# Performance work log

Hardware: AMD Instinct MI355X
Metric: run time of the kernel (lower is better)

The kernel has to match this reference:

```python
import jax, jax.numpy as jnp
import numpy as np

B = 16384       # batch of weight blocks
IN = 64         # input_size == e_dim
DENC = 512      # dim_encoder
NRES = 2        # n_resblock (weights shared, see ResidualStack [block]*n)
NE = 2048       # n_embeddings
P = 12          # basis vectors per block
BETA = 0.25
SCALE = 1.0
SHIFT = 0.0


def setup_inputs() -> dict:
    key = jax.random.key(0)
    ks = jax.random.split(key, 6)
    s = 0.02
    return {
        "x": jax.random.normal(ks[0], (B, IN), dtype=jnp.float32),
        "enc_w1": jax.random.normal(ks[1], (IN, DENC), dtype=jnp.float32) * s,
        "enc_b1": jnp.zeros((DENC,), jnp.float32),
        "res_w": jax.random.normal(ks[2], (DENC, DENC), dtype=jnp.float32) * s,
        "res_b": jnp.zeros((DENC,), jnp.float32),
        "res_g": jnp.ones((DENC,), jnp.float32),
        "res_beta": jnp.zeros((DENC,), jnp.float32),
        "enc_w2": jax.random.normal(ks[3], (DENC, IN * P), dtype=jnp.float32) * s,
        "enc_b2": jnp.zeros((IN * P,), jnp.float32),
        "emb": jax.random.uniform(ks[4], (NE, IN), jnp.float32, -1.0 / NE, 1.0 / NE),
    }


def _layer_norm(r, g, b):
    mu = jnp.mean(r, axis=-1, keepdims=True)
    var = jnp.mean((r - mu) ** 2, axis=-1, keepdims=True)
    return (r - mu) * jax.lax.rsqrt(var + 1e-5) * g + b


def reference(x, enc_w1, enc_b1, res_w, res_b, res_g, res_beta, enc_w2, enc_b2, emb):
    sg = jax.lax.stop_gradient
    x_shift = (x - SHIFT) / SCALE

    # encoder: Linear -> (shared ResBlock) x NRES -> Linear
    h = x_shift @ enc_w1 + enc_b1                      # (B, DENC)
    for _ in range(NRES):
        h = h + jax.nn.relu(_layer_norm(h @ res_w + res_b, res_g, res_beta))
    z = h @ enc_w2 + enc_b2                            # (B, P*IN)

    z_e = z.reshape(B, P, IN)
    zf = z_e.reshape(-1, IN)                           # (B*P, IN)

    # pairwise squared distances to codebook, argmin, gather
    d = (jnp.sum(zf ** 2, axis=1, keepdims=True)
         + jnp.sum(emb ** 2, axis=1)
         - 2.0 * zf @ emb.T)                           # (B*P, NE)
    idx = jnp.argmin(d, axis=1)                        # (B*P,)
    z_q = emb[idx].reshape(B, P, IN)

    loss = (jnp.mean((sg(z_q) - z_e) ** 2)
            + BETA * jnp.mean((z_q - sg(z_e)) ** 2))

    # straight-through estimator
    z_q = z_e + sg(z_q - z_e)

    counts = jnp.zeros((NE,), jnp.float32).at[idx].add(1.0) / idx.shape[0]
    perplexity = jnp.exp(-jnp.sum(counts * jnp.log(counts + 1e-10)))

    # pinv-based reconstruction: A (B, IN, P), coeff = pinv(A) @ x_shift
    A = jnp.transpose(z_q, (0, 2, 1))                  # (B, IN, P)
    coeff = jnp.matmul(jnp.linalg.pinv(A), x_shift[..., None])  # (B, P, 1)
    x_hat = jnp.matmul(A, coeff)[..., 0]               # (B, IN)
    x_hat = SCALE * x_hat + SHIFT

    return (loss, x_hat, perplexity, idx, coeff)
```

## Files before the change

kernel.cpp:

```cpp
#include <hip/hip_runtime.h>
#include <math.h>

#define B_    16384
#define IN_   64
#define DENC_ 512
#define NE_   2048
#define P_    12
#define ROWS_ 196608
#define BETA_ 0.25

#define XHAT_OFF 1
#define PERP_OFF 1048577
#define IDXF_OFF 1048578
#define COEF_OFF 1245186

typedef __bf16 bf16x8 __attribute__((ext_vector_type(8)));
typedef float  f32x16 __attribute__((ext_vector_type(16)));

__device__ __forceinline__ void split3(float v, __bf16& h, __bf16& m, __bf16& l) {
    h = (__bf16)v;
    float r1 = v - (float)h;
    m = (__bf16)r1;
    float r2 = r1 - (float)m;
    l = (__bf16)r2;
}

__global__ void k_wsplit(const float* __restrict__ W,
                         __bf16* __restrict__ Wh, __bf16* __restrict__ Wm,
                         __bf16* __restrict__ Wl, int kshift, int N, int total) {
    int idx = blockIdx.x * 256 + threadIdx.x;
    if (idx < total) {
        int n = idx >> kshift;
        int k = idx & ((1 << kshift) - 1);
        float v = W[(size_t)k * N + n];
        __bf16 h, m, l;
        split3(v, h, m, l);
        Wh[idx] = h; Wm[idx] = m; Wl[idx] = l;
    }
}

__global__ __launch_bounds__(256) void k_gemm_mfma(const float* __restrict__ A,
                                                   const __bf16* __restrict__ Bh,
                                                   const __bf16* __restrict__ Bm,
                                                   const __bf16* __restrict__ Bl,
                                                   const float* __restrict__ bias,
                                                   float* __restrict__ C,
                                                   int N, int K) {
    __shared__ __bf16 eS[3][64 * 64];

    const int tid = threadIdx.x;
    const int w = tid >> 6, lane = tid & 63;
    const int r0 = blockIdx.y * 128 + w * 32;
    const int n0 = blockIdx.x * 64;
    const int lrow = lane & 31;
    const int half = lane >> 5;

    f32x16 acc0, acc1;
#pragma unroll
    for (int i = 0; i < 16; ++i) { acc0[i] = 0.0f; acc1[i] = 0.0f; }

    for (int k0 = 0; k0 < K; k0 += 64) {
        __syncthreads();
        {
            const int col = tid >> 3, q = tid & 7;
#pragma unroll
            for (int p = 0; p < 2; ++p) {
                int cc = col + 32 * p;
                int g = q ^ (cc & 7);
                size_t soff = (size_t)(n0 + cc) * K + k0 + q * 8;
                int doff = cc * 64 + g * 8;
                *(float4*)(&eS[0][doff]) = *(const float4*)(Bh + soff);
                *(float4*)(&eS[1][doff]) = *(const float4*)(Bm + soff);
                *(float4*)(&eS[2][doff]) = *(const float4*)(Bl + soff);
            }
        }
        __syncthreads();

        bf16x8 ah[4], am[4], al[4];
        {
            const float* ar = A + (size_t)(r0 + lrow) * K + k0 + half * 8;
#pragma unroll
            for (int kc = 0; kc < 4; ++kc) {
                float4 u0 = *(const float4*)(ar + kc * 16);
                float4 u1 = *(const float4*)(ar + kc * 16 + 4);
                float v[8] = {u0.x, u0.y, u0.z, u0.w, u1.x, u1.y, u1.z, u1.w};
#pragma unroll
                for (int j = 0; j < 8; ++j) {
                    __bf16 hh, mm, ll;
                    split3(v[j], hh, mm, ll);
                    ah[kc][j] = hh; am[kc][j] = mm; al[kc][j] = ll;
                }
            }
        }

#pragma unroll
        for (int kc = 0; kc < 4; ++kc) {
            const int q = kc * 2 + half;
            const int g = (q ^ (lrow & 7)) * 8;
            bf16x8 b0h = *(const bf16x8*)(&eS[0][lrow * 64 + g]);
            bf16x8 b0m = *(const bf16x8*)(&eS[1][lrow * 64 + g]);
            bf16x8 b0l = *(const bf16x8*)(&eS[2][lrow * 64 + g]);
            bf16x8 b1h = *(const bf16x8*)(&eS[0][(lrow + 32) * 64 + g]);
            bf16x8 b1m = *(const bf16x8*)(&eS[1][(lrow + 32) * 64 + g]);
            bf16x8 b1l = *(const bf16x8*)(&eS[2][(lrow + 32) * 64 + g]);

            acc0 = __builtin_amdgcn_mfma_f32_32x32x16_bf16(ah[kc], b0h, acc0, 0, 0, 0);
            acc1 = __builtin_amdgcn_mfma_f32_32x32x16_bf16(ah[kc], b1h, acc1, 0, 0, 0);
            acc0 = __builtin_amdgcn_mfma_f32_32x32x16_bf16(ah[kc], b0m, acc0, 0, 0, 0);
            acc1 = __builtin_amdgcn_mfma_f32_32x32x16_bf16(ah[kc], b1m, acc1, 0, 0, 0);
            acc0 = __builtin_amdgcn_mfma_f32_32x32x16_bf16(am[kc], b0h, acc0, 0, 0, 0);
            acc1 = __builtin_amdgcn_mfma_f32_32x32x16_bf16(am[kc], b1h, acc1, 0, 0, 0);
            acc0 = __builtin_amdgcn_mfma_f32_32x32x16_bf16(ah[kc], b0l, acc0, 0, 0, 0);
            acc1 = __builtin_amdgcn_mfma_f32_32x32x16_bf16(ah[kc], b1l, acc1, 0, 0, 0);
            acc0 = __builtin_amdgcn_mfma_f32_32x32x16_bf16(am[kc], b0m, acc0, 0, 0, 0);
            acc1 = __builtin_amdgcn_mfma_f32_32x32x16_bf16(am[kc], b1m, acc1, 0, 0, 0);
            acc0 = __builtin_amdgcn_mfma_f32_32x32x16_bf16(al[kc], b0h, acc0, 0, 0, 0);
            acc1 = __builtin_amdgcn_mfma_f32_32x32x16_bf16(al[kc], b1h, acc1, 0, 0, 0);
        }
    }

    const int col0 = n0 + lrow, col1 = col0 + 32;
    const float bv0 = bias[col0], bv1 = bias[col1];
#pragma unroll
    for (int r = 0; r < 16; ++r) {
        int row = r0 + (r & 3) + 8 * (r >> 2) + 4 * half;
        C[(size_t)row * N + col0] = acc0[r] + bv0;
        C[(size_t)row * N + col1] = acc1[r] + bv1;
    }
}

__global__ __launch_bounds__(256) void k_lnrelu(const float* __restrict__ t,
                                                float* __restrict__ h,
                                                const float* __restrict__ g,
                                                const float* __restrict__ beta) {
    const int tid = threadIdx.x;
    const int wv = tid >> 6, lane = tid & 63;
    const int row = blockIdx.x * 4 + wv;
    const float* tr = t + (size_t)row * DENC_;
    float* hr = h + (size_t)row * DENC_;

    float4 v0 = *(const float4*)(tr + lane * 4);
    float4 v1 = *(const float4*)(tr + 256 + lane * 4);

    float s = v0.x + v0.y + v0.z + v0.w + v1.x + v1.y + v1.z + v1.w;
#pragma unroll
    for (int m = 1; m < 64; m <<= 1) s += __shfl_xor(s, m);
    float mu = s / 512.0f;

    float d0x = v0.x - mu, d0y = v0.y - mu, d0z = v0.z - mu, d0w = v0.w - mu;
    float d1x = v1.x - mu, d1y = v1.y - mu, d1z = v1.z - mu, d1w = v1.w - mu;
    float vs = d0x * d0x + d0y * d0y + d0z * d0z + d0w * d0w +
               d1x * d1x + d1y * d1y + d1z * d1z + d1w * d1w;
#pragma unroll
    for (int m = 1; m < 64; m <<= 1) vs += __shfl_xor(vs, m);
    float var = vs / 512.0f;
    float rs = (float)(1.0 / sqrt((double)var + 1e-5));

    float4 g0 = *(const float4*)(g + lane * 4);
    float4 g1 = *(const float4*)(g + 256 + lane * 4);
    float4 b0 = *(const float4*)(beta + lane * 4);
    float4 b1 = *(const float4*)(beta + 256 + lane * 4);

    float4 h0 = *(float4*)(hr + lane * 4);
    float4 h1 = *(float4*)(hr + 256 + lane * 4);

    h0.x += fmaxf(d0x * rs * g0.x + b0.x, 0.0f);
    h0.y += fmaxf(d0y * rs * g0.y + b0.y, 0.0f);
    h0.z += fmaxf(d0z * rs * g0.z + b0.z, 0.0f);
    h0.w += fmaxf(d0w * rs * g0.w + b0.w, 0.0f);
    h1.x += fmaxf(d1x * rs * g1.x + b1.x, 0.0f);
    h1.y += fmaxf(d1y * rs * g1.y + b1.y, 0.0f);
    h1.z += fmaxf(d1z * rs * g1.z + b1.z, 0.0f);
    h1.w += fmaxf(d1w * rs * g1.w + b1.w, 0.0f);

    *(float4*)(hr + lane * 4) = h0;
    *(float4*)(hr + 256 + lane * 4) = h1;
}

__global__ void k_esplit(const float* __restrict__ emb, float* __restrict__ se,
                         __bf16* __restrict__ Ehi, __bf16* __restrict__ Emid,
                         __bf16* __restrict__ Elo) {
    int c = blockIdx.x * 256 + threadIdx.x;
    if (c < NE_) {
        float s = 0.0f;
        for (int k = 0; k < 64; ++k) {
            float v = emb[(size_t)c * 64 + k];
            s += v * v;
            __bf16 h, m, l;
            split3(v, h, m, l);
            Ehi[(size_t)c * 64 + k] = h;
            Emid[(size_t)c * 64 + k] = m;
            Elo[(size_t)c * 64 + k] = l;
        }
        se[c] = s;
    }
}

__global__ __launch_bounds__(256) void k_rowsq(const float* __restrict__ z,
                                               float* __restrict__ sz) {
    const int tid = threadIdx.x;
    const int row = blockIdx.x * 64 + (tid >> 2);
    const int part = tid & 3;
    const float4* zp = (const float4*)(z + (size_t)row * 64) + part * 4;
    float s = 0.0f;
#pragma unroll
    for (int i = 0; i < 4; ++i) {
        float4 v = zp[i];
        s += v.x * v.x + v.y * v.y + v.z * v.z + v.w * v.w;
    }
    s += __shfl_xor(s, 1);
    s += __shfl_xor(s, 2);
    if (part == 0) sz[row] = s;
}

__global__ __launch_bounds__(256) void k_distm(const float* __restrict__ z,
                                               const float* __restrict__ se,
                                               const float* __restrict__ sz,
                                               const __bf16* __restrict__ Ehi,
                                               const __bf16* __restrict__ Emid,
                                               const __bf16* __restrict__ Elo,
                                               int* __restrict__ idxw,
                                               float* __restrict__ idxf,
                                               float* __restrict__ dminw,
                                               int* __restrict__ counts) {
    __shared__ __bf16 eS[3][64 * 64];

    const int tid = threadIdx.x;
    const int w = tid >> 6, lane = tid & 63;
    const int r0 = blockIdx.x * 128 + w * 32;
    const int lrow = lane & 31;
    const int half = lane >> 5;

    bf16x8 ah[4], am[4], al[4];
    {
        const float* zr = z + (size_t)(r0 + lrow) * 64 + half * 8;
#pragma unroll
        for (int kc = 0; kc < 4; ++kc) {
            float4 u0 = *(const float4*)(zr + kc * 16);
            float4 u1 = *(const float4*)(zr + kc * 16 + 4);
            float v[8] = {u0.x, u0.y, u0.z, u0.w, u1.x, u1.y, u1.z, u1.w};
#pragma unroll
            for (int j = 0; j < 8; ++j) {
                __bf16 hh, mm, ll;
                split3(v[j], hh, mm, ll);
                ah[kc][j] = hh; am[kc][j] = mm; al[kc][j] = ll;
            }
        }
    }

    float szv[16];
#pragma unroll
    for (int r = 0; r < 16; ++r) {
        int rl = (r & 3) + 8 * (r >> 2) + 4 * half;
        szv[r] = sz[r0 + rl];
    }

    float bd[16];
    int bi[16];
#pragma unroll
    for (int r = 0; r < 16; ++r) { bd[r] = 1e30f; bi[r] = 0; }

    for (int ch = 0; ch < 32; ++ch) {
        const int c0 = ch * 64;
        __syncthreads();
        {
            const int col = tid >> 3, q = tid & 7;
#pragma unroll
            for (int p = 0; p < 2; ++p) {
                int cc = col + 32 * p;
                int g = q ^ (cc & 7);
                size_t soff = (size_t)(c0 + cc) * 64 + q * 8;
                int doff = cc * 64 + g * 8;
                *(float4*)(&eS[0][doff]) = *(const float4*)(Ehi + soff);
                *(float4*)(&eS[1][doff]) = *(const float4*)(Emid + soff);
                *(float4*)(&eS[2][doff]) = *(const float4*)(Elo + soff);
            }
        }
        __syncthreads();

        f32x16 acc0, acc1;
#pragma unroll
        for (int i = 0; i < 16; ++i) { acc0[i] = 0.0f; acc1[i] = 0.0f; }

#pragma unroll
        for (int kc = 0; kc < 4; ++kc) {
            const int q = kc * 2 + half;
            const int g = (q ^ (lrow & 7)) * 8;
            bf16x8 b0h = *(const bf16x8*)(&eS[0][lrow * 64 + g]);
            bf16x8 b0m = *(const bf16x8*)(&eS[1][lrow * 64 + g]);
            bf16x8 b0l = *(const bf16x8*)(&eS[2][lrow * 64 + g]);
            bf16x8 b1h = *(const bf16x8*)(&eS[0][(lrow + 32) * 64 + g]);
            bf16x8 b1m = *(const bf16x8*)(&eS[1][(lrow + 32) * 64 + g]);
            bf16x8 b1l = *(const bf16x8*)(&eS[2][(lrow + 32) * 64 + g]);

            acc0 = __builtin_amdgcn_mfma_f32_32x32x16_bf16(ah[kc], b0h, acc0, 0, 0, 0);
            acc1 = __builtin_amdgcn_mfma_f32_32x32x16_bf16(ah[kc], b1h, acc1, 0, 0, 0);
            acc0 = __builtin_amdgcn_mfma_f32_32x32x16_bf16(ah[kc], b0m, acc0, 0, 0, 0);
            acc1 = __builtin_amdgcn_mfma_f32_32x32x16_bf16(ah[kc], b1m, acc1, 0, 0, 0);
            acc0 = __builtin_amdgcn_mfma_f32_32x32x16_bf16(am[kc], b0h, acc0, 0, 0, 0);
            acc1 = __builtin_amdgcn_mfma_f32_32x32x16_bf16(am[kc], b1h, acc1, 0, 0, 0);
            acc0 = __builtin_amdgcn_mfma_f32_32x32x16_bf16(ah[kc], b0l, acc0, 0, 0, 0);
            acc1 = __builtin_amdgcn_mfma_f32_32x32x16_bf16(ah[kc], b1l, acc1, 0, 0, 0);
            acc0 = __builtin_amdgcn_mfma_f32_32x32x16_bf16(am[kc], b0m, acc0, 0, 0, 0);
            acc1 = __builtin_amdgcn_mfma_f32_32x32x16_bf16(am[kc], b1m, acc1, 0, 0, 0);
            acc0 = __builtin_amdgcn_mfma_f32_32x32x16_bf16(al[kc], b0h, acc0, 0, 0, 0);
            acc1 = __builtin_amdgcn_mfma_f32_32x32x16_bf16(al[kc], b1h, acc1, 0, 0, 0);
        }

        const float se0 = se[c0 + lrow];
        const float se1 = se[c0 + lrow + 32];
        const int   ci0 = c0 + lrow, ci1 = c0 + lrow + 32;
#pragma unroll
        for (int r = 0; r < 16; ++r) {
            float d0 = fmaf(-2.0f, acc0[r], szv[r] + se0);
            if (d0 < bd[r]) { bd[r] = d0; bi[r] = ci0; }
            float d1 = fmaf(-2.0f, acc1[r], szv[r] + se1);
            if (d1 < bd[r]) { bd[r] = d1; bi[r] = ci1; }
        }
    }

#pragma unroll
    for (int r = 0; r < 16; ++r) {
        float d = bd[r];
        int i = bi[r];
#pragma unroll
        for (int off = 1; off < 32; off <<= 1) {
            float od = __shfl_xor(d, off);
            int oi = __shfl_xor(i, off);
            if (od < d || (od == d && oi < i)) { d = od; i = oi; }
        }
        bd[r] = d; bi[r] = i;
    }

    if (lrow == 0) {
#pragma unroll
        for (int r = 0; r < 16; ++r) {
            int rl = (r & 3) + 8 * (r >> 2) + 4 * half;
            int row = r0 + rl;
            idxw[row] = bi[r];
            idxf[row] = (float)bi[r];
            dminw[row] = bd[r];
            atomicAdd(&counts[bi[r]], 1);
        }
    }
}

__global__ __launch_bounds__(1024) void k_lossperp(const float* __restrict__ dmin,
                                                   const int* __restrict__ counts,
                                                   float* __restrict__ out) {
    __shared__ double red[1024];
    const int tid = threadIdx.x;

    double s = 0.0;
    for (int i = tid; i < ROWS_; i += 1024) s += (double)dmin[i];
    red[tid] = s;
    __syncthreads();
    for (int off = 512; off > 0; off >>= 1) {
        if (tid < off) red[tid] += red[tid + off];
        __syncthreads();
    }
    if (tid == 0) out[0] = (float)(red[0] * (1.0 + BETA_) / ((double)ROWS_ * IN_));
    __syncthreads();

    double hsum = 0.0;
    for (int i = tid; i < NE_; i += 1024) {
        float p = (float)counts[i] / 196608.0f;
        float lg = logf(p + 1e-10f);
        hsum += (double)(p * lg);
    }
    red[tid] = hsum;
    __syncthreads();
    for (int off = 512; off > 0; off >>= 1) {
        if (tid < off) red[tid] += red[tid + off];
        __syncthreads();
    }
    if (tid == 0) out[PERP_OFF] = (float)exp(-red[0]);
}

__global__ __launch_bounds__(256) void k_pinv(const float* __restrict__ xin,
                                              const float* __restrict__ emb,
                                              const int* __restrict__ idxw,
                                              float* __restrict__ coeff,
                                              float* __restrict__ xhat) {
    __shared__ float aS[4][12][65];
    __shared__ float xS[4][64];
    __shared__ double GS[4][12][12];
    __shared__ double bS[4][12];
    __shared__ double uS[4][12];
    __shared__ float cS[4][12];

    const int tid = threadIdx.x;
    const int wv = tid >> 6, lane = tid & 63;
    const int b = blockIdx.x * 4 + wv;

    int my = 0;
    if (lane < 12) my = idxw[(size_t)b * 12 + lane];
    int id[12];
#pragma unroll
    for (int p = 0; p < 12; ++p) id[p] = __shfl(my, p);

    int rep = lane, mcnt = 1;
    if (lane < 12) {
        rep = -1;
        mcnt = 0;
        for (int q = 0; q < 12; ++q) {
            if (id[q] == id[lane]) {
                if (rep < 0) rep = q;
                mcnt++;
            }
        }
    }

#pragma unroll
    for (int p = 0; p < 12; ++p) aS[wv][p][lane] = emb[(size_t)id[p] * 64 + lane];
    xS[wv][lane] = xin[(size_t)b * 64 + lane];
    __syncthreads();

    for (int item = lane; item < 90; item += 64) {
        if (item < 78) {
            int j = 0, k = 0, c = item;
            for (j = 0; j < 12; ++j) {
                int cnt = 12 - j;
                if (c < cnt) { k = j + c; break; }
                c -= cnt;
            }
            double s = 0.0;
            for (int t = 0; t < 64; ++t) s += (double)aS[wv][j][t] * (double)aS[wv][k][t];
            GS[wv][j][k] = s;
            GS[wv][k][j] = s;
        } else {
            int j = item - 78;
            double s = 0.0;
            for (int t = 0; t < 64; ++t) s += (double)aS[wv][j][t] * (double)xS[wv][t];
            bS[wv][j] = s;
        }
    }
    __syncthreads();

    if (lane == 0) {
        for (int p = 0; p < 12; ++p) {
            int rp = -1;
            for (int q = 0; q < 12; ++q) {
                if (id[q] == id[p]) { rp = q; break; }
            }
            if (rp != p) {
                for (int q = 0; q < 12; ++q) {
                    GS[wv][p][q] = 0.0;
                    GS[wv][q][p] = 0.0;
                }
                GS[wv][p][p] = 1.0;
                bS[wv][p] = 0.0;
            }
        }
    }
    __syncthreads();

    for (int j = 0; j < 12; ++j) {
        if (lane == j) {
            double s = GS[wv][j][j];
            for (int k = 0; k < j; ++k) {
                double l = GS[wv][j][k];
                s -= l * l;
            }
            GS[wv][j][j] = sqrt(fmax(s, 1e-30));
        }
        __syncthreads();
        if (lane > j && lane < 12) {
            double s = GS[wv][lane][j];
            for (int k = 0; k < j; ++k) s -= GS[wv][lane][k] * GS[wv][j][k];
            GS[wv][lane][j] = s / GS[wv][j][j];
        }
        __syncthreads();
    }

    if (lane == 0) {
        double y[12];
        for (int i = 0; i < 12; ++i) {
            double s = bS[wv][i];
            for (int k = 0; k < i; ++k) s -= GS[wv][i][k] * y[k];
            y[i] = s / GS[wv][i][i];
        }
        for (int i = 11; i >= 0; --i) {
            double s = y[i];
            for (int k = i + 1; k < 12; ++k) s -= GS[wv][k][i] * uS[wv][k];
            uS[wv][i] = s / GS[wv][i][i];
        }
    }
    __syncthreads();

    if (lane < 12) {
        double c = uS[wv][rep] / (double)mcnt;
        coeff[(size_t)b * 12 + lane] = (float)c;
        cS[wv][lane] = (float)c;
    }
    __syncthreads();

    float s = 0.0f;
#pragma unroll
    for (int p = 0; p < 12; ++p) s += aS[wv][p][lane] * cS[wv][p];
    xhat[(size_t)b * 64 + lane] = s;
}


extern "C" void kernel_launch(void* const* d_in, const int* in_sizes, int n_in,
                              void* d_out, int out_size, void* d_ws, size_t ws_size,
                              hipStream_t stream) {
    const float* x        = (const float*)d_in[0];
    const float* enc_w1   = (const float*)d_in[1];
    const float* enc_b1   = (const float*)d_in[2];
    const float* res_w    = (const float*)d_in[3];
    const float* res_b    = (const float*)d_in[4];
    const float* res_g    = (const float*)d_in[5];
    const float* res_beta = (const float*)d_in[6];
    const float* enc_w2   = (const float*)d_in[7];
    const float* enc_b2   = (const float*)d_in[8];
    const float* emb      = (const float*)d_in[9];

    float* out = (float*)d_out;

    float* h  = (float*)d_ws;
    float* tz = h + (size_t)B_ * DENC_;
    float* se    = h;
    float* sz    = h + 2048;
    float* dmin  = h + 2048 + (size_t)ROWS_;
    int*   idxw  = (int*)(h + 2048 + 2 * (size_t)ROWS_);
    int*   cnts  = (int*)(h + 2048 + 3 * (size_t)ROWS_);
    __bf16* Ehi  = (__bf16*)(h + 2048 + 3 * (size_t)ROWS_ + 2048);
    __bf16* Emid = Ehi + (size_t)NE_ * 64;
    __bf16* Elo  = Emid + (size_t)NE_ * 64;
    __bf16* W1h = (__bf16*)(tz + (size_t)B_ * 768);
    __bf16* W1m = W1h + (size_t)DENC_ * IN_;
    __bf16* W1l = W1m + (size_t)DENC_ * IN_;
    __bf16* Wrh = W1l + (size_t)DENC_ * IN_;
    __bf16* Wrm = Wrh + (size_t)DENC_ * DENC_;
    __bf16* Wrl = Wrm + (size_t)DENC_ * DENC_;
    __bf16* W2h = Wrl + (size_t)DENC_ * DENC_;
    __bf16* W2m = W2h + (size_t)768 * DENC_;
    __bf16* W2l = W2m + (size_t)768 * DENC_;

    float* t = tz;
    float* z = tz;

    k_wsplit<<<(DENC_ * IN_ + 255) / 256, 256, 0, stream>>>(enc_w1, W1h, W1m, W1l, 6, DENC_, DENC_ * IN_);
    k_wsplit<<<(DENC_ * DENC_ + 255) / 256, 256, 0, stream>>>(res_w, Wrh, Wrm, Wrl, 9, DENC_, DENC_ * DENC_);
    k_wsplit<<<(768 * DENC_ + 255) / 256, 256, 0, stream>>>(enc_w2, W2h, W2m, W2l, 9, 768, 768 * DENC_);

    k_gemm_mfma<<<dim3(DENC_ / 64, B_ / 128), 256, 0, stream>>>(x, W1h, W1m, W1l, enc_b1, h, DENC_, IN_);
    for (int r = 0; r < 2; ++r) {
        k_gemm_mfma<<<dim3(DENC_ / 64, B_ / 128), 256, 0, stream>>>(h, Wrh, Wrm, Wrl, res_b, t, DENC_, DENC_);
        k_lnrelu<<<B_ / 4, 256, 0, stream>>>(t, h, res_g, res_beta);
    }
    k_gemm_mfma<<<dim3(768 / 64, B_ / 128), 256, 0, stream>>>(h, W2h, W2m, W2l, enc_b2, z, 768, DENC_);

    hipMemsetAsync(cnts, 0, NE_ * sizeof(int), stream);
    k_esplit<<<NE_ / 256, 256, 0, stream>>>(emb, se, Ehi, Emid, Elo);
    k_rowsq<<<ROWS_ / 64, 256, 0, stream>>>(z, sz);
    k_distm<<<ROWS_ / 128, 256, 0, stream>>>(z, se, sz, Ehi, Emid, Elo,
                                             idxw, out + IDXF_OFF, dmin, cnts);
    k_lossperp<<<1, 1024, 0, stream>>>(dmin, cnts, out);
    k_pinv<<<B_ / 4, 256, 0, stream>>>(x, emb, idxw, out + COEF_OFF, out + XHAT_OFF);
}
```

Baseline: 776.3 us.

## Pre-split GEMM activations to bf16 triples and double-buffer weight tiles via direct LDS loads

Activations are now split into hi/mid/lo bf16 arrays by a separate kernel before each encoder GEMM, instead of every N-tile block redoing the fp32 split. The GEMM double-buffers the weight tiles in LDS using global_load_lds and prefetches the next K-chunk while computing the current one, which drops one barrier per iteration. The codebook split is also parallelised per element and separated from the squared-norm pass. In exchange there are extra kernel launches and extra global traffic for the split activation buffers, and LDS use per block doubles.

```diff
diff --git a/kernel.cpp b/kernel.cpp
--- a/kernel.cpp
+++ b/kernel.cpp
@@ -23,6 +23,11 @@
     m = (__bf16)r1;
     float r2 = r1 - (float)m;
     l = (__bf16)r2;
+}
+
+__device__ __forceinline__ void gload_lds16(const void* g, void* l) {
+    __builtin_amdgcn_global_load_lds((const __attribute__((address_space(1))) void*)g,
+                                     (__attribute__((address_space(3))) void*)l, 16, 0, 0);
 }
 
 __global__ void k_wsplit(const float* __restrict__ W,
@@ -39,14 +44,35 @@
     }
 }
 
-__global__ __launch_bounds__(256) void k_gemm_mfma(const float* __restrict__ A,
+__global__ __launch_bounds__(256) void k_asplit(const float* __restrict__ A,
+                                                __bf16* __restrict__ Ah,
+                                                __bf16* __restrict__ Am,
+                                                __bf16* __restrict__ Al,
+                                                int total4) {
+    int i4 = blockIdx.x * 256 + threadIdx.x;
+    if (i4 < total4) {
+        float4 v = *(const float4*)(A + (size_t)i4 * 4);
+        __bf16 h[4], m[4], l[4];
+        split3(v.x, h[0], m[0], l[0]);
+        split3(v.y, h[1], m[1], l[1]);
+        split3(v.z, h[2], m[2], l[2]);
+        split3(v.w, h[3], m[3], l[3]);
+        *(short4*)(Ah + (size_t)i4 * 4) = *(short4*)h;
+        *(short4*)(Am + (size_t)i4 * 4) = *(short4*)m;
+        *(short4*)(Al + (size_t)i4 * 4) = *(short4*)l;
+    }
+}
+
+__global__ __launch_bounds__(256) void k_gemm_mfma(const __bf16* __restrict__ Ah,
+                                                   const __bf16* __restrict__ Am,
+                                                   const __bf16* __restrict__ Al,
                                                    const __bf16* __restrict__ Bh,
                                                    const __bf16* __restrict__ Bm,
                                                    const __bf16* __restrict__ Bl,
                                                    const float* __restrict__ bias,
                                                    float* __restrict__ C,
                                                    int N, int K) {
-    __shared__ __bf16 eS[3][64 * 64];
+    __shared__ __bf16 eS[2][3][64 * 64];
 
     const int tid = threadIdx.x;
     const int w = tid >> 6, lane = tid & 63;
@@ -55,41 +81,52 @@
     const int lrow = lane & 31;
     const int half = lane >> 5;
 
+    const int cc0 = tid >> 3, qq = tid & 7;
+    const int cc1 = cc0 + 32;
+    const size_t off0 = (size_t)cc0 * K + (size_t)((qq ^ (cc0 & 7)) * 8);
+    const size_t off1 = (size_t)cc1 * K + (size_t)((qq ^ (cc1 & 7)) * 8);
+    const size_t nbase = (size_t)n0 * K;
+    const int ld0 = w * 512;
+    const int ld1 = 2048 + w * 512;
+
     f32x16 acc0, acc1;
 #pragma unroll
     for (int i = 0; i < 16; ++i) { acc0[i] = 0.0f; acc1[i] = 0.0f; }
 
-    for (int k0 = 0; k0 < K; k0 += 64) {
+    {
+        const size_t b = nbase;
+        gload_lds16(Bh + b + off0, &eS[0][0][ld0]);
+        gload_lds16(Bh + b + off1, &eS[0][0][ld1]);
+        gload_lds16(Bm + b + off0, &eS[0][1][ld0]);
+        gload_lds16(Bm + b + off1, &eS[0][1][ld1]);
+        gload_lds16(Bl + b + off0, &eS[0][2][ld0]);
+        gload_lds16(Bl + b + off1, &eS[0][2][ld1]);
+    }
+
+    const int nch = K >> 6;
+    for (int ch = 0; ch < nch; ++ch) {
+        const int cur = ch & 1;
         __syncthreads();
-        {
-            const int col = tid >> 3, q = tid & 7;
-#pragma unroll
-            for (int p = 0; p < 2; ++p) {
-                int cc = col + 32 * p;
-                int g = q ^ (cc & 7);
-                size_t soff = (size_t)(n0 + cc) * K + k0 + q * 8;
-                int doff = cc * 64 + g * 8;
-                *(float4*)(&eS[0][doff]) = *(const float4*)(Bh + soff);
-                *(float4*)(&eS[1][doff]) = *(const float4*)(Bm + soff);
-                *(float4*)(&eS[2][doff]) = *(const float4*)(Bl + soff);
-            }
-        }
-        __syncthreads();
+
+        if (ch + 1 < nch) {
+            const int nxt = cur ^ 1;
+            const size_t b = nbase + (size_t)(ch + 1) * 64;
+            gload_lds16(Bh + b + off0, &eS[nxt][0][ld0]);
+            gload_lds16(Bh + b + off1, &eS[nxt][0][ld1]);
+            gload_lds16(Bm + b + off0, &eS[nxt][1][ld0]);
+            gload_lds16(Bm + b + off1, &eS[nxt][1][ld1]);
+            gload_lds16(Bl + b + off0, &eS[nxt][2][ld0]);
+            gload_lds16(Bl + b + off1, &eS[nxt][2][ld1]);
+        }
 
         bf16x8 ah[4], am[4], al[4];
         {
-            const float* ar = A + (size_t)(r0 + lrow) * K + k0 + half * 8;
+            const size_t abase = (size_t)(r0 + lrow) * K + ch * 64 + half * 8;
 #pragma unroll
             for (int kc = 0; kc < 4; ++kc) {
-                float4 u0 = *(const float4*)(ar + kc * 16);
-                float4 u1 = *(const float4*)(ar + kc * 16 + 4);
-                float v[8] = {u0.x, u0.y, u0.z, u0.w, u1.x, u1.y, u1.z, u1.w};
-#pragma unroll
-                for (int j = 0; j < 8; ++j) {
-                    __bf16 hh, mm, ll;
-                    split3(v[j], hh, mm, ll);
-                    ah[kc][j] = hh; am[kc][j] = mm; al[kc][j] = ll;
-                }
+                ah[kc] = *(const bf16x8*)(Ah + abase + kc * 16);
+                am[kc] = *(const bf16x8*)(Am + abase + kc * 16);
+                al[kc] = *(const bf16x8*)(Al + abase + kc * 16);
             }
         }
 
@@ -97,12 +134,12 @@
         for (int kc = 0; kc < 4; ++kc) {
             const int q = kc * 2 + half;
             const int g = (q ^ (lrow & 7)) * 8;
-            bf16x8 b0h = *(const bf16x8*)(&eS[0][lrow * 64 + g]);
-            bf16x8 b0m = *(const bf16x8*)(&eS[1][lrow * 64 + g]);
-            bf16x8 b0l = *(const bf16x8*)(&eS[2][lrow * 64 + g]);
-            bf16x8 b1h = *(const bf16x8*)(&eS[0][(lrow + 32) * 64 + g]);
-            bf16x8 b1m = *(const bf16x8*)(&eS[1][(lrow + 32) * 64 + g]);
-            bf16x8 b1l = *(const bf16x8*)(&eS[2][(lrow + 32) * 64 + g]);
+            bf16x8 b0h = *(const bf16x8*)(&eS[cur][0][lrow * 64 + g]);
+            bf16x8 b0m = *(const bf16x8*)(&eS[cur][1][lrow * 64 + g]);
+            bf16x8 b0l = *(const bf16x8*)(&eS[cur][2][lrow * 64 + g]);
+            bf16x8 b1h = *(const bf16x8*)(&eS[cur][0][(lrow + 32) * 64 + g]);
+            bf16x8 b1m = *(const bf16x8*)(&eS[cur][1][(lrow + 32) * 64 + g]);
+            bf16x8 b1l = *(const bf16x8*)(&eS[cur][2][(lrow + 32) * 64 + g]);
 
             acc0 = __builtin_amdgcn_mfma_f32_32x32x16_bf16(ah[kc], b0h, acc0, 0, 0, 0);
             acc1 = __builtin_amdgcn_mfma_f32_32x32x16_bf16(ah[kc], b1h, acc1, 0, 0, 0);
@@ -177,22 +214,29 @@
     *(float4*)(hr + 256 + lane * 4) = h1;
 }
 
-__global__ void k_esplit(const float* __restrict__ emb, float* __restrict__ se,
-                         __bf16* __restrict__ Ehi, __bf16* __restrict__ Emid,
-                         __bf16* __restrict__ Elo) {
-    int c = blockIdx.x * 256 + threadIdx.x;
-    if (c < NE_) {
+__global__ __launch_bounds__(256) void k_esplit_fast(const float* __restrict__ emb,
+                                                     __bf16* __restrict__ Ehi,
+                                                     __bf16* __restrict__ Emid,
+                                                     __bf16* __restrict__ Elo) {
+    const int wv = threadIdx.x >> 6, lane = threadIdx.x & 63;
+    const int c = blockIdx.x * 4 + wv;
+    float v = emb[(size_t)c * 64 + lane];
+    __bf16 h, m, l;
+    split3(v, h, m, l);
+    Ehi[(size_t)c * 64 + lane] = h;
+    Emid[(size_t)c * 64 + lane] = m;
+    Elo[(size_t)c * 64 + lane] = l;
+}
+
+__global__ void k_esq(const float* __restrict__ emb, float* __restrict__ se) {
+    int t = blockIdx.x * 256 + threadIdx.x;
+    if (t < NE_) {
         float s = 0.0f;
         for (int k = 0; k < 64; ++k) {
-            float v = emb[(size_t)c * 64 + k];
+            float v = emb[(size_t)t * 64 + k];
             s += v * v;
-            __bf16 h, m, l;
-            split3(v, h, m, l);
-            Ehi[(size_t)c * 64 + k] = h;
-            Emid[(size_t)c * 64 + k] = m;
-            Elo[(size_t)c * 64 + k] = l;
-        }
-        se[c] = s;
+        }
+        se[t] = s;
     }
 }
 
@@ -537,6 +581,12 @@
     __bf16* W2h = Wrl + (size_t)DENC_ * DENC_;
     __bf16* W2m = W2h + (size_t)768 * DENC_;
     __bf16* W2l = W2m + (size_t)768 * DENC_;
+    __bf16* Xh = W2l + (size_t)768 * DENC_;
+    __bf16* Xm = Xh + (size_t)B_ * IN_;
+    __bf16* Xl = Xm + (size_t)B_ * IN_;
+    __bf16* Hh = Xl + (size_t)B_ * IN_;
+    __bf16* Hm = Hh + (size_t)B_ * DENC_;
+    __bf16* Hl = Hm + (size_t)B_ * DENC_;
 
     float* t = tz;
     float* z = tz;
@@ -545,15 +595,19 @@
     k_wsplit<<<(DENC_ * DENC_ + 255) / 256, 256, 0, stream>>>(res_w, Wrh, Wrm, Wrl, 9, DENC_, DENC_ * DENC_);
     k_wsplit<<<(768 * DENC_ + 255) / 256, 256, 0, stream>>>(enc_w2, W2h, W2m, W2l, 9, 768, 768 * DENC_);
 
-    k_gemm_mfma<<<dim3(DENC_ / 64, B_ / 128), 256, 0, stream>>>(x, W1h, W1m, W1l, enc_b1, h, DENC_, IN_);
+    k_asplit<<<(B_ * IN_ / 4 + 255) / 256, 256, 0, stream>>>(x, Xh, Xm, Xl, B_ * IN_ / 4);
+    k_gemm_mfma<<<dim3(DENC_ / 64, B_ / 128), 256, 0, stream>>>(Xh, Xm, Xl, W1h, W1m, W1l, enc_b1, h, DENC_, IN_);
     for (int r = 0; r < 2; ++r) {
-        k_gemm_mfma<<<dim3(DENC_ / 64, B_ / 128), 256, 0, stream>>>(h, Wrh, Wrm, Wrl, res_b, t, DENC_, DENC_);
+        k_asplit<<<(B_ * DENC_ / 4 + 255) / 256, 256, 0, stream>>>(h, Hh, Hm, Hl, B_ * DENC_ / 4);
+        k_gemm_mfma<<<dim3(DENC_ / 64, B_ / 128), 256, 0, stream>>>(Hh, Hm, Hl, Wrh, Wrm, Wrl, res_b, t, DENC_, DENC_);
         k_lnrelu<<<B_ / 4, 256, 0, stream>>>(t, h, res_g, res_beta);
     }
-    k_gemm_mfma<<<dim3(768 / 64, B_ / 128), 256, 0, stream>>>(h, W2h, W2m, W2l, enc_b2, z, 768, DENC_);
+    k_asplit<<<(B_ * DENC_ / 4 + 255) / 256, 256, 0, stream>>>(h, Hh, Hm, Hl, B_ * DENC_ / 4);
+    k_gemm_mfma<<<dim3(768 / 64, B_ / 128), 256, 0, stream>>>(Hh, Hm, Hl, W2h, W2m, W2l, enc_b2, z, 768, DENC_);
 
     hipMemsetAsync(cnts, 0, NE_ * sizeof(int), stream);
-    k_esplit<<<NE_ / 256, 256, 0, stream>>>(emb, se, Ehi, Emid, Elo);
+    k_esplit_fast<<<NE_ / 4, 256, 0, stream>>>(emb, Ehi, Emid, Elo);
+    k_esq<<<NE_ / 256, 256, 0, stream>>>(emb, se);
     k_rowsq<<<ROWS_ / 64, 256, 0, stream>>>(z, sz);
     k_distm<<<ROWS_ / 128, 256, 0, stream>>>(z, se, sz, Ehi, Emid, Elo,
                                              idxw, out + IDXF_OFF, dmin, cnts);
```

Measured after the change: 898.6 us. 1.16x slower.
